# Optimization experiments

Hardware: AMD Instinct MI355X
Metric: run time of the kernel (lower is better)

Reference implementation:

```python
import jax, jax.numpy as jnp
import numpy as np

BETA = 0.8  # decay hyperparameter from __init__


def setup_inputs() -> dict:
    key = jax.random.key(0)
    k1, k2, k3 = jax.random.split(key, 3)
    N = 1048576   # total messages in batch (with duplicate node ids)
    D = 256       # message_length
    S = 65536     # number of node-id segments
    node_ids = jax.random.randint(k1, (N,), 0, S)
    messages = jax.random.normal(k2, (N, D), dtype=jnp.float32)
    # timestamps: positive event times; within-group spread drives the exp decay
    timestamps = jax.random.uniform(k3, (N,), dtype=jnp.float32) * 10000.0
    return {"messages": messages, "timestamps": timestamps,
            "node_ids": node_ids, "num_segments": S}


def reference(messages, timestamps, node_ids, num_segments):
    # last timestamp per node (segment max); empty segments get -inf, never indexed
    last_t = jax.ops.segment_max(timestamps, node_ids, num_segments=num_segments)
    # exp-decay weights relative to each node's most recent timestamp
    w = jnp.exp(BETA * (timestamps - last_t[node_ids]))          # [N]
    wsum = jax.ops.segment_sum(messages * w[:, None], node_ids,
                               num_segments=num_segments)        # [S, D]
    tw = jax.ops.segment_sum(w, node_ids, num_segments=num_segments)  # [S]
    # total_weight > 0 for every non-empty group (max element has weight 1);
    # empty groups produce zeros (original simply skips them)
    agg = jnp.where(tw[:, None] > 0, wsum / jnp.maximum(tw, 1e-30)[:, None], 0.0)
    last_t_out = jnp.where(tw > 0, last_t, 0.0)
    return agg, last_t_out
```

## Files before the change

### kernel.cpp

```cpp
#include <hip/hip_runtime.h>

#define BETA 0.8f
#define D 256
#define SCAN_T 1024

__global__ void hist_kernel(const int* __restrict__ node,
                            int* __restrict__ counts, int N) {
    int i = blockIdx.x * blockDim.x + threadIdx.x;
    if (i < N) atomicAdd(&counts[node[i]], 1);
}

__global__ void scan_kernel(const int* __restrict__ counts,
                            int* __restrict__ offsets,
                            int* __restrict__ cursor, int S) {
    __shared__ int sums[SCAN_T];
    int tid   = threadIdx.x;
    int chunk = (S + SCAN_T - 1) / SCAN_T;
    int base  = tid * chunk;

    int s = 0;
    for (int i = 0; i < chunk; ++i) {
        int j = base + i;
        if (j < S) s += counts[j];
    }
    sums[tid] = s;
    __syncthreads();

    for (int off = 1; off < SCAN_T; off <<= 1) {
        int v = 0;
        if (tid >= off) v = sums[tid - off];
        __syncthreads();
        if (tid >= off) sums[tid] += v;
        __syncthreads();
    }

    int run = (tid > 0) ? sums[tid - 1] : 0;
    for (int i = 0; i < chunk; ++i) {
        int j = base + i;
        if (j < S) {
            offsets[j] = run;
            cursor[j]  = run;
            run += counts[j];
        }
    }
}

__global__ void scatter_kernel(const int* __restrict__ node,
                               int* __restrict__ cursor,
                               int* __restrict__ sorted, int N) {
    int i = blockIdx.x * blockDim.x + threadIdx.x;
    if (i < N) {
        int pos = atomicAdd(&cursor[node[i]], 1);
        sorted[pos] = i;
    }
}

__global__ void reduce_kernel(const float* __restrict__ msgs,
                              const float* __restrict__ ts,
                              const int* __restrict__ sorted,
                              const int* __restrict__ offsets,
                              const int* __restrict__ counts,
                              float* __restrict__ agg,
                              float* __restrict__ last_t_out,
                              int S) {
    int gid  = blockIdx.x * blockDim.x + threadIdx.x;
    int seg  = gid >> 6;
    int lane = threadIdx.x & 63;
    if (seg >= S) return;

    float4* orow = (float4*)(agg + (size_t)seg * D);
    int cnt = counts[seg];
    if (cnt == 0) {
        orow[lane] = make_float4(0.f, 0.f, 0.f, 0.f);
        if (lane == 0) last_t_out[seg] = 0.0f;
        return;
    }
    int start = offsets[seg];

    float maxt = -1e30f;
    for (int r = 0; r < cnt; ++r) {
        int idx = sorted[start + r];
        maxt = fmaxf(maxt, ts[idx]);
    }

    float4 acc = make_float4(0.f, 0.f, 0.f, 0.f);
    float  tw  = 0.0f;
    for (int r = 0; r < cnt; ++r) {
        int   idx = sorted[start + r];
        float w   = __expf(BETA * (ts[idx] - maxt));
        const float4* row = (const float4*)(msgs + (size_t)idx * D);
        float4 m = row[lane];
        acc.x += m.x * w;
        acc.y += m.y * w;
        acc.z += m.z * w;
        acc.w += m.w * w;
        tw    += w;
    }

    float inv = 1.0f / tw;
    orow[lane] = make_float4(acc.x * inv, acc.y * inv, acc.z * inv, acc.w * inv);
    if (lane == 0) last_t_out[seg] = maxt;
}

extern "C" void kernel_launch(void* const* d_in, const int* in_sizes, int n_in,
                              void* d_out, int out_size, void* d_ws, size_t ws_size,
                              hipStream_t stream) {
    const float* msgs = (const float*)d_in[0];
    const float* ts   = (const float*)d_in[1];
    const int*   node = (const int*)d_in[2];
    const int N = in_sizes[1];
    const int S = out_size / (D + 1);

    float* agg        = (float*)d_out;
    float* last_t_out = (float*)d_out + (size_t)S * D;

    int* counts  = (int*)d_ws;
    int* offsets = counts + S;
    int* cursor  = offsets + S;
    int* sorted  = cursor + S;

    hipMemsetAsync(counts, 0, (size_t)S * sizeof(int), stream);

    hist_kernel<<<(N + 255) / 256, 256, 0, stream>>>(node, counts, N);
    scan_kernel<<<1, SCAN_T, 0, stream>>>(counts, offsets, cursor, S);
    scatter_kernel<<<(N + 255) / 256, 256, 0, stream>>>(node, cursor, sorted, N);

    long long threads = (long long)S * 64;
    reduce_kernel<<<(int)((threads + 255) / 256), 256, 0, stream>>>(
        msgs, ts, sorted, offsets, counts, agg, last_t_out, S);
}
```

Baseline: 1.700 ms.

## Co-sort timestamps and cooperatively load indices/weights per wavefront with shuffle broadcast

The scatter pass now writes each message's timestamp into a sorted_t array next to its index. The reduce kernel then reads timestamps contiguously instead of gathering them through the index. Each lane loads one index and one weight per 64-row tile, and these are broadcast with shuffles, replacing the old serial loads that every lane repeated. The max and weight-sum become wavefront reductions, and the row gather loop is unrolled by four for more memory-level parallelism. In exchange this needs extra workspace for sorted_t and adds shuffle traffic.

```diff
diff --git a/kernel.cpp b/kernel.cpp
--- a/kernel.cpp
+++ b/kernel.cpp
@@ -46,18 +46,21 @@
 }
 
 __global__ void scatter_kernel(const int* __restrict__ node,
+                               const float* __restrict__ ts,
                                int* __restrict__ cursor,
-                               int* __restrict__ sorted, int N) {
+                               int* __restrict__ sorted,
+                               float* __restrict__ sorted_t, int N) {
     int i = blockIdx.x * blockDim.x + threadIdx.x;
     if (i < N) {
         int pos = atomicAdd(&cursor[node[i]], 1);
-        sorted[pos] = i;
+        sorted[pos]   = i;
+        sorted_t[pos] = ts[i];
     }
 }
 
 __global__ void reduce_kernel(const float* __restrict__ msgs,
-                              const float* __restrict__ ts,
                               const int* __restrict__ sorted,
+                              const float* __restrict__ sorted_t,
                               const int* __restrict__ offsets,
                               const int* __restrict__ counts,
                               float* __restrict__ agg,
@@ -77,29 +80,60 @@
     }
     int start = offsets[seg];
 
-    float maxt = -1e30f;
-    for (int r = 0; r < cnt; ++r) {
-        int idx = sorted[start + r];
-        maxt = fmaxf(maxt, ts[idx]);
+    float tmax = -1e30f;
+    for (int base = 0; base < cnt; base += 64) {
+        int r = base + lane;
+        float t = (r < cnt) ? sorted_t[start + r] : -1e30f;
+        tmax = fmaxf(tmax, t);
     }
+    #pragma unroll
+    for (int off = 32; off > 0; off >>= 1)
+        tmax = fmaxf(tmax, __shfl_xor(tmax, off));
 
     float4 acc = make_float4(0.f, 0.f, 0.f, 0.f);
     float  tw  = 0.0f;
-    for (int r = 0; r < cnt; ++r) {
-        int   idx = sorted[start + r];
-        float w   = __expf(BETA * (ts[idx] - maxt));
-        const float4* row = (const float4*)(msgs + (size_t)idx * D);
-        float4 m = row[lane];
-        acc.x += m.x * w;
-        acc.y += m.y * w;
-        acc.z += m.z * w;
-        acc.w += m.w * w;
-        tw    += w;
+    for (int base = 0; base < cnt; base += 64) {
+        int r    = base + lane;
+        int tile = cnt - base; if (tile > 64) tile = 64;
+
+        int   idx = 0;
+        float w   = 0.0f;
+        if (r < cnt) {
+            idx = sorted[start + r];
+            w   = __expf(BETA * (sorted_t[start + r] - tmax));
+            tw += w;
+        }
+
+        int j = 0;
+        for (; j + 4 <= tile; j += 4) {
+            int   i0 = __shfl(idx, j),     i1 = __shfl(idx, j + 1);
+            int   i2 = __shfl(idx, j + 2), i3 = __shfl(idx, j + 3);
+            float w0 = __shfl(w, j),       w1 = __shfl(w, j + 1);
+            float w2 = __shfl(w, j + 2),   w3 = __shfl(w, j + 3);
+            float4 m0 = ((const float4*)(msgs + (size_t)i0 * D))[lane];
+            float4 m1 = ((const float4*)(msgs + (size_t)i1 * D))[lane];
+            float4 m2 = ((const float4*)(msgs + (size_t)i2 * D))[lane];
+            float4 m3 = ((const float4*)(msgs + (size_t)i3 * D))[lane];
+            acc.x += m0.x * w0; acc.y += m0.y * w0; acc.z += m0.z * w0; acc.w += m0.w * w0;
+            acc.x += m1.x * w1; acc.y += m1.y * w1; acc.z += m1.z * w1; acc.w += m1.w * w1;
+            acc.x += m2.x * w2; acc.y += m2.y * w2; acc.z += m2.z * w2; acc.w += m2.w * w2;
+            acc.x += m3.x * w3; acc.y += m3.y * w3; acc.z += m3.z * w3; acc.w += m3.w * w3;
+        }
+        for (; j < tile; ++j) {
+            int   ib = __shfl(idx, j);
+            float wb = __shfl(w, j);
+            float4 m = ((const float4*)(msgs + (size_t)ib * D))[lane];
+            acc.x += m.x * wb; acc.y += m.y * wb; acc.z += m.z * wb; acc.w += m.w * wb;
+        }
     }
+
+    #pragma unroll
+    for (int off = 32; off > 0; off >>= 1)
+        tw += __shfl_xor(tw, off);
 
     float inv = 1.0f / tw;
     orow[lane] = make_float4(acc.x * inv, acc.y * inv, acc.z * inv, acc.w * inv);
-    if (lane == 0) last_t_out[seg] = maxt;
+    if (lane == 0) last_t_out[seg] = tmax;
 }
 
 extern "C" void kernel_launch(void* const* d_in, const int* in_sizes, int n_in,
@@ -114,18 +148,20 @@
     float* agg        = (float*)d_out;
     float* last_t_out = (float*)d_out + (size_t)S * D;
 
-    int* counts  = (int*)d_ws;
-    int* offsets = counts + S;
-    int* cursor  = offsets + S;
-    int* sorted  = cursor + S;
+    int*   counts   = (int*)d_ws;
+    int*   offsets  = counts + S;
+    int*   cursor   = offsets + S;
+    int*   sorted   = cursor + S;
+    float* sorted_t = (float*)(sorted + N);
 
     hipMemsetAsync(counts, 0, (size_t)S * sizeof(int), stream);
 
     hist_kernel<<<(N + 255) / 256, 256, 0, stream>>>(node, counts, N);
     scan_kernel<<<1, SCAN_T, 0, stream>>>(counts, offsets, cursor, S);
-    scatter_kernel<<<(N + 255) / 256, 256, 0, stream>>>(node, cursor, sorted, N);
+    scatter_kernel<<<(N + 255) / 256, 256, 0, stream>>>(node, ts, cursor,
+                                                        sorted, sorted_t, N);
 
     long long threads = (long long)S * 64;
     reduce_kernel<<<(int)((threads + 255) / 256), 256, 0, stream>>>(
-        msgs, ts, sorted, offsets, counts, agg, last_t_out, S);
+        msgs, sorted, sorted_t, offsets, counts, agg, last_t_out, S);
 }
```

New measurement: 1.625 ms. -4.4%, faster.
